# Kernel tuning notes

Hardware: AMD Instinct MI355X
Metric: run time of the kernel (lower is better)

The kernel has to match this reference:

```python
import jax, jax.numpy as jnp
import numpy as np

IN_DIM, MEM_DIM, NUM_WORDS, N_LEAVES = 300, 256, 50000, 8192


def setup_inputs() -> dict:
    key = jax.random.key(0)
    ks = jax.random.split(key, 6)
    s = 0.05
    return {
        "embs": jax.random.normal(ks[0], (N_LEAVES, IN_DIM), jnp.float32),
        "Wx": jax.random.normal(ks[1], (4 * MEM_DIM, IN_DIM), jnp.float32) * s,
        "bx": jax.random.normal(ks[2], (4 * MEM_DIM,), jnp.float32) * s,
        "Wl": jax.random.normal(ks[3], (5 * MEM_DIM, MEM_DIM), jnp.float32) * s,
        "Wr": jax.random.normal(ks[4], (5 * MEM_DIM, MEM_DIM), jnp.float32) * s,
        "emb_table": jax.random.normal(ks[5], (NUM_WORDS, IN_DIM), jnp.float32),
    }


def reference(embs, Wx, bx, Wl, Wr, emb_table):
    m = Wl.shape[1]

    # x-projection order along fused axis: [cx, ix, fx, ox]
    def proj_x(x):  # [B, in] -> [B, 4, m]
        return (x @ Wx.T + bx).reshape(x.shape[0], 4, m)

    # hidden-projection order: [u, i, lf, rf, o]
    def compose(xg, lc, lh, rc, rh):
        lg = (lh @ Wl.T).reshape(-1, 5, m)
        rg = (rh @ Wr.T).reshape(-1, 5, m)
        u = jnp.tanh(xg[:, 0] + lg[:, 0] + rg[:, 0])
        i = jax.nn.sigmoid(xg[:, 1] + lg[:, 1] + rg[:, 1])
        lf = jax.nn.sigmoid(xg[:, 2] + lg[:, 2] + rg[:, 2])  # fx shared
        rf = jax.nn.sigmoid(xg[:, 2] + lg[:, 3] + rg[:, 3])  # fx shared
        c = i * u + lf * lc + rf * rc
        o = jax.nn.sigmoid(xg[:, 3] + lg[:, 4] + rg[:, 4])
        h = o * jnp.tanh(c)
        return c, h

    # leaves: zero child states, per-leaf embedding inputs
    L = embs.shape[0]
    z = jnp.zeros((L, m), embs.dtype)
    c, h = compose(proj_x(embs), z, z, z, z)

    # internal nodes (PAD=True): input is word_embedding(num_words - 1)
    pad_xg = proj_x(emb_table[-1:])  # [1, 4, m]

    while c.shape[0] > 1:  # static shapes; 13 merge levels
        lc, rc = c[0::2], c[1::2]
        lh, rh = h[0::2], h[1::2]
        B = lc.shape[0]
        c, h = compose(jnp.broadcast_to(pad_xg, (B, 4, m)), lc, lh, rc, rh)

    return jnp.stack([c, h])  # root (c, h): [2, 1, mem_dim]
```

## Files before the change

kernel.cpp:

```cpp
#include <hip/hip_runtime.h>
#include <hip/hip_bf16.h>
#include <math.h>


#define MEM 256

typedef __attribute__((ext_vector_type(8))) short bf16x8;
typedef __attribute__((ext_vector_type(4))) float f32x4;

__device__ __forceinline__ float sigf(float x) { return 1.0f / (1.0f + __expf(-x)); }

__device__ __forceinline__ unsigned short f2b(float f) {
  unsigned int u = __float_as_uint(f);
  u = (u + 0x7FFFu + ((u >> 16) & 1u)) >> 16;
  return (unsigned short)u;
}

__device__ __forceinline__ unsigned short cvt1(float f) {
  __hip_bfloat16 b = __float2bfloat16(f);
  return *reinterpret_cast<unsigned short*>(&b);
}

__device__ __forceinline__ bf16x8 gather8(const float* __restrict__ rowp, int k0) {
  bf16x8 r;
  if (k0 + 8 <= 300) {
    const float4 f0 = *(const float4*)(rowp + k0);
    const float4 f1 = *(const float4*)(rowp + k0 + 4);
    r[0] = cvt1(f0.x); r[1] = cvt1(f0.y); r[2] = cvt1(f0.z); r[3] = cvt1(f0.w);
    r[4] = cvt1(f1.x); r[5] = cvt1(f1.y); r[6] = cvt1(f1.z); r[7] = cvt1(f1.w);
  } else {
#pragma unroll
    for (int j = 0; j < 8; j++) {
      int k = k0 + j;
      r[j] = (k < 300) ? (short)cvt1(rowp[k]) : (short)0;
    }
  }
  return r;
}

#define NB_LEAF 1024
#define NB_WCF 2560
__global__ __launch_bounds__(256) void k_fused(
    const float* __restrict__ embs, const float* __restrict__ Wx,
    const float* __restrict__ bx, const float* __restrict__ Wl,
    const float* __restrict__ Wr, const float* __restrict__ emb_last,
    unsigned short* __restrict__ Wcf, float* __restrict__ bias5,
    float* __restrict__ cO, unsigned short* __restrict__ hO) {
  int b = blockIdx.x;
  int tid = threadIdx.x;
  if (b < NB_LEAF) {
    int grp = b & 15, rblk = b >> 4;
    int lane = tid & 63, wave = tid >> 6;
    int tb = (rblk * 4 + wave) * 2;
    int m = lane & 15, quad = lane >> 4;
    const int gmap[3] = {0, 1, 3};

    f32x4 acc[2][3];
#pragma unroll
    for (int rt = 0; rt < 2; rt++)
#pragma unroll
      for (int g = 0; g < 3; g++) acc[rt][g] = (f32x4){0.f, 0.f, 0.f, 0.f};

    const float* ar0 = embs + (tb * 16 + m) * 300;
    const float* ar1 = embs + ((tb + 1) * 16 + m) * 300;
    const float* wr0 = Wx + (gmap[0] * 256 + grp * 16 + m) * 300;
    const float* wr1 = Wx + (gmap[1] * 256 + grp * 16 + m) * 300;
    const float* wr2 = Wx + (gmap[2] * 256 + grp * 16 + m) * 300;
#pragma unroll
    for (int kc = 0; kc < 10; kc++) {
      int k0 = kc * 32 + quad * 8;
      bf16x8 a0 = gather8(ar0, k0);
      bf16x8 a1 = gather8(ar1, k0);
      bf16x8 w0 = gather8(wr0, k0);
      acc[0][0] = __builtin_amdgcn_mfma_f32_16x16x32_bf16(a0, w0, acc[0][0], 0, 0, 0);
      acc[1][0] = __builtin_amdgcn_mfma_f32_16x16x32_bf16(a1, w0, acc[1][0], 0, 0, 0);
      bf16x8 w1 = gather8(wr1, k0);
      acc[0][1] = __builtin_amdgcn_mfma_f32_16x16x32_bf16(a0, w1, acc[0][1], 0, 0, 0);
      acc[1][1] = __builtin_amdgcn_mfma_f32_16x16x32_bf16(a1, w1, acc[1][1], 0, 0, 0);
      bf16x8 w2 = gather8(wr2, k0);
      acc[0][2] = __builtin_amdgcn_mfma_f32_16x16x32_bf16(a0, w2, acc[0][2], 0, 0, 0);
      acc[1][2] = __builtin_amdgcn_mfma_f32_16x16x32_bf16(a1, w2, acc[1][2], 0, 0, 0);
    }
    int col = grp * 16 + m;
    float b0 = bx[col], b1 = bx[256 + col], b3 = bx[768 + col];
#pragma unroll
    for (int rt = 0; rt < 2; rt++) {
#pragma unroll
      for (int reg = 0; reg < 4; reg++) {
        int row = (tb + rt) * 16 + quad * 4 + reg;
        float u = tanhf(acc[rt][0][reg] + b0);
        float ig = sigf(acc[rt][1][reg] + b1);
        float o = sigf(acc[rt][2][reg] + b3);
        float c = ig * u;
        cO[row * MEM + col] = c;
        hO[row * MEM + col] = f2b(o * tanhf(c));
      }
    }
  } else if (b < NB_LEAF + NB_WCF) {
    int idx = (b - NB_LEAF) * 256 + tid;
    int f = idx >> 9, r = idx & 511;
    int lane = r >> 3, j = r & 7;
    int gate = f % 5, t = f / 5;
    int grp = t & 15, kc = t >> 4;
    int k = kc * 32 + ((lane >> 4) << 3) + j;
    int n = gate * 256 + (grp << 4) + (lane & 15);
    float v = (k < 256) ? Wl[n * 256 + k] : Wr[n * 256 + (k - 256)];
    Wcf[idx] = f2b(v);
  } else {
    int g = b - (NB_LEAF + NB_WCF);
    __shared__ float er[300];
    for (int k = tid; k < 300; k += 256) er[k] = emb_last[k];
    __syncthreads();
    const int map[5] = {0, 1, 2, 2, 3};
    int wrow = map[g] * 256 + tid;
    const float* w = Wx + wrow * 300;
    float s = bx[wrow];
    for (int k = 0; k < 300; k++) s += er[k] * w[k];
    bias5[g * 256 + tid] = s;
  }
}

template <int RT>
__global__ __launch_bounds__(256) void k_compose_mfma(
    const unsigned short* __restrict__ hprev,
    const float* __restrict__ cprev,
    const unsigned short* __restrict__ Wcf, const float* __restrict__ bias5,
    float* __restrict__ cO, unsigned short* __restrict__ hO,
    float* __restrict__ hOf, int B) {
  int lane = threadIdx.x & 63;
  int wave = threadIdx.x >> 6;
  int grp = blockIdx.y;
  int tb = (blockIdx.x * 4 + wave) * RT;
  if (tb * 16 >= B) return;
  int m = lane & 15, quad = lane >> 4;
  const bf16x8 zz = {0, 0, 0, 0, 0, 0, 0, 0};

  f32x4 acc[RT][5];
  const unsigned short* ar[RT];
  bool ok[RT];
#pragma unroll
  for (int rt = 0; rt < RT; rt++) {
    int ra = (tb + rt) * 16 + m;
    ok[rt] = (ra < B);
    ar[rt] = hprev + ra * 512 + quad * 8;
#pragma unroll
    for (int g = 0; g < 5; g++) acc[rt][g] = (f32x4){0.f, 0.f, 0.f, 0.f};
  }

#pragma unroll
  for (int kc = 0; kc < 16; kc++) {
    const unsigned short* bp = Wcf + ((kc * 16 + grp) * 5) * 512 + lane * 8;
    bf16x8 b0 = *(const bf16x8*)(bp);
    bf16x8 b1 = *(const bf16x8*)(bp + 512);
    bf16x8 b2 = *(const bf16x8*)(bp + 1024);
    bf16x8 b3 = *(const bf16x8*)(bp + 1536);
    bf16x8 b4 = *(const bf16x8*)(bp + 2048);
#pragma unroll
    for (int rt = 0; rt < RT; rt++) {
      bf16x8 a = ok[rt] ? *(const bf16x8*)(ar[rt] + kc * 32) : zz;
      acc[rt][0] = __builtin_amdgcn_mfma_f32_16x16x32_bf16(a, b0, acc[rt][0], 0, 0, 0);
      acc[rt][1] = __builtin_amdgcn_mfma_f32_16x16x32_bf16(a, b1, acc[rt][1], 0, 0, 0);
      acc[rt][2] = __builtin_amdgcn_mfma_f32_16x16x32_bf16(a, b2, acc[rt][2], 0, 0, 0);
      acc[rt][3] = __builtin_amdgcn_mfma_f32_16x16x32_bf16(a, b3, acc[rt][3], 0, 0, 0);
      acc[rt][4] = __builtin_amdgcn_mfma_f32_16x16x32_bf16(a, b4, acc[rt][4], 0, 0, 0);
    }
  }
  int col = grp * 16 + m;
  float b0 = bias5[col], b1 = bias5[256 + col], b2 = bias5[512 + col];
  float b3 = bias5[768 + col], b4 = bias5[1024 + col];
#pragma unroll
  for (int rt = 0; rt < RT; rt++) {
#pragma unroll
    for (int reg = 0; reg < 4; reg++) {
      int row = (tb + rt) * 16 + quad * 4 + reg;
      if (row >= B) continue;
      float u = tanhf(acc[rt][0][reg] + b0);
      float ig = sigf(acc[rt][1][reg] + b1);
      float lf = sigf(acc[rt][2][reg] + b2);
      float rf = sigf(acc[rt][3][reg] + b3);
      float o = sigf(acc[rt][4][reg] + b4);
      float lc = cprev[(2 * row) * MEM + col];
      float rc = cprev[(2 * row + 1) * MEM + col];
      float c = ig * u + lf * lc + rf * rc;
      float h = o * tanhf(c);
      cO[row * MEM + col] = c;
      hO[row * MEM + col] = f2b(h);
      if (hOf) hOf[row * MEM + col] = h;
    }
  }
}

__global__ __launch_bounds__(256) void k_compose_ksplit(
    const unsigned short* __restrict__ hprev, const float* __restrict__ cprev,
    const unsigned short* __restrict__ Wcf, const float* __restrict__ bias5,
    float* __restrict__ cO, unsigned short* __restrict__ hO,
    float* __restrict__ hOf, int B) {
  __shared__ __align__(16) float lds[4 * 2 * 5 * 64 * 4];
  int tid = threadIdx.x;
  int lane = tid & 63, wave = tid >> 6;
  int grp = blockIdx.y;
  int m = lane & 15, quad = lane >> 4;
  int tiles = (B + 15) >> 4;
  const bf16x8 zz = {0, 0, 0, 0, 0, 0, 0, 0};

  f32x4 acc[2][5];
  bool ok[2];
  const unsigned short* ar[2];
#pragma unroll
  for (int t = 0; t < 2; t++) {
    int ra = t * 16 + m;
    ok[t] = (t < tiles) && (ra < B);
    ar[t] = hprev + ra * 512 + quad * 8;
#pragma unroll
    for (int q = 0; q < 5; q++) acc[t][q] = (f32x4){0.f, 0.f, 0.f, 0.f};
  }

#pragma unroll
  for (int kcl = 0; kcl < 4; kcl++) {
    int kc = wave * 4 + kcl;
    const unsigned short* bp = Wcf + ((kc * 16 + grp) * 5) * 512 + lane * 8;
    bf16x8 b0 = *(const bf16x8*)(bp);
    bf16x8 b1 = *(const bf16x8*)(bp + 512);
    bf16x8 b2 = *(const bf16x8*)(bp + 1024);
    bf16x8 b3 = *(const bf16x8*)(bp + 1536);
    bf16x8 b4 = *(const bf16x8*)(bp + 2048);
#pragma unroll
    for (int t = 0; t < 2; t++) {
      if (t < tiles) {
        bf16x8 a = ok[t] ? *(const bf16x8*)(ar[t] + kc * 32) : zz;
        acc[t][0] = __builtin_amdgcn_mfma_f32_16x16x32_bf16(a, b0, acc[t][0], 0, 0, 0);
        acc[t][1] = __builtin_amdgcn_mfma_f32_16x16x32_bf16(a, b1, acc[t][1], 0, 0, 0);
        acc[t][2] = __builtin_amdgcn_mfma_f32_16x16x32_bf16(a, b2, acc[t][2], 0, 0, 0);
        acc[t][3] = __builtin_amdgcn_mfma_f32_16x16x32_bf16(a, b3, acc[t][3], 0, 0, 0);
        acc[t][4] = __builtin_amdgcn_mfma_f32_16x16x32_bf16(a, b4, acc[t][4], 0, 0, 0);
      }
    }
  }
#pragma unroll
  for (int t = 0; t < 2; t++)
    if (t < tiles)
#pragma unroll
      for (int q = 0; q < 5; q++)
        *(f32x4*)&lds[(((wave * 2 + t) * 5 + q) * 64 + lane) * 4] = acc[t][q];
  __syncthreads();

  if (wave < tiles) {
    int t = wave;
    int col = grp * 16 + m;
    float b0 = bias5[col], b1 = bias5[256 + col], b2 = bias5[512 + col];
    float b3 = bias5[768 + col], b4 = bias5[1024 + col];
    f32x4 s[5];
#pragma unroll
    for (int q = 0; q < 5; q++) {
      s[q] = *(const f32x4*)&lds[(((0 * 2 + t) * 5 + q) * 64 + lane) * 4];
#pragma unroll
      for (int v = 1; v < 4; v++) {
        f32x4 p = *(const f32x4*)&lds[(((v * 2 + t) * 5 + q) * 64 + lane) * 4];
        s[q][0] += p[0]; s[q][1] += p[1]; s[q][2] += p[2]; s[q][3] += p[3];
      }
    }
#pragma unroll
    for (int reg = 0; reg < 4; reg++) {
      int row = t * 16 + quad * 4 + reg;
      if (row >= B) continue;
      float u = tanhf(s[0][reg] + b0);
      float ig = sigf(s[1][reg] + b1);
      float lf = sigf(s[2][reg] + b2);
      float rf = sigf(s[3][reg] + b3);
      float o = sigf(s[4][reg] + b4);
      float lc = cprev[(2 * row) * MEM + col];
      float rc = cprev[(2 * row + 1) * MEM + col];
      float c = ig * u + lf * lc + rf * rc;
      float h = o * tanhf(c);
      cO[row * MEM + col] = c;
      hO[row * MEM + col] = f2b(h);
      if (hOf) hOf[row * MEM + col] = h;
    }
  }
}

extern "C" void kernel_launch(void* const* d_in, const int* in_sizes, int n_in,
                              void* d_out, int out_size, void* d_ws, size_t ws_size,
                              hipStream_t stream) {
  const float* embs = (const float*)d_in[0];
  const float* Wx = (const float*)d_in[1];
  const float* bx = (const float*)d_in[2];
  const float* Wl = (const float*)d_in[3];
  const float* Wr = (const float*)d_in[4];
  const float* emb_table = (const float*)d_in[5];
  float* out = (float*)d_out;

  float* ws = (float*)d_ws;
  float* cA = ws;
  float* cB = cA + 8192 * 256;
  float* bias5 = cB + 4096 * 256;
  unsigned short* hA = (unsigned short*)(bias5 + 1280);
  unsigned short* hB = hA + 8192 * 256;
  unsigned short* Wcf = hB + 4096 * 256;

  k_fused<<<NB_LEAF + NB_WCF + 5, 256, 0, stream>>>(
      embs, Wx, bx, Wl, Wr, emb_table + (in_sizes[5] - 300),
      Wcf, bias5, cA, hA);

  const float* cs = cA;
  const unsigned short* hs = hA;
  int B = 4096;
  int lvl = 0;
  while (B >= 1) {
    float* dc;
    unsigned short* dh;
    float* dhf = nullptr;
    if (B == 1) {
      dc = out;
      dh = hB;
      dhf = out + 256;
    } else if ((lvl & 1) == 0) {
      dc = cB; dh = hB;
    } else {
      dc = cA; dh = hA;
    }
    int tiles = (B + 15) / 16;
    if (B == 4096) {
      k_compose_mfma<2><<<dim3(tiles / 8, 16), 256, 0, stream>>>(
          hs, cs, Wcf, bias5, dc, dh, dhf, B);
    } else if (B >= 64) {
      int gx = (tiles + 3) / 4;
      k_compose_mfma<1><<<dim3(gx, 16), 256, 0, stream>>>(
          hs, cs, Wcf, bias5, dc, dh, dhf, B);
    } else {
      k_compose_ksplit<<<dim3(1, 16), 256, 0, stream>>>(
          hs, cs, Wcf, bias5, dc, dh, dhf, B);
    }
    cs = dc;
    hs = dh;
    B >>= 1;
    lvl++;
  }
}
```

Measured before the change: 265.1 us.

## Pre-convert leaf embeddings and Wx to bf16 fragments, split leaf GEMM kernel, remap block order

The prep kernel now converts embs to a padded bf16 buffer and Wx into MFMA-fragment order, and a separate leaf kernel consumes these with plain vector loads. This replaces the per-block fp32 gather-and-convert, which repeated the conversion of each weight row across many blocks. The Wcf conversion is vectorized to 8 elements per thread. Compose kernels switch to a 1D grid with a sliced block-to-tile remap, likely aimed at cache or XCD locality. The cost is an extra launch plus an extra round trip through memory for the bf16 embedding copy.

Result: faster. 249.3 us (-6.0%).

```diff
diff --git a/kernel.cpp b/kernel.cpp
--- a/kernel.cpp
+++ b/kernel.cpp
@@ -1,5 +1,4 @@
 #include <hip/hip_runtime.h>
-#include <hip/hip_bf16.h>
 #include <math.h>
 
 
@@ -16,98 +15,65 @@
   return (unsigned short)u;
 }
 
-__device__ __forceinline__ unsigned short cvt1(float f) {
-  __hip_bfloat16 b = __float2bfloat16(f);
-  return *reinterpret_cast<unsigned short*>(&b);
-}
-
-__device__ __forceinline__ bf16x8 gather8(const float* __restrict__ rowp, int k0) {
+__device__ __forceinline__ bf16x8 c8(const float* __restrict__ p) {
+  float4 f0 = *(const float4*)(p);
+  float4 f1 = *(const float4*)(p + 4);
   bf16x8 r;
-  if (k0 + 8 <= 300) {
-    const float4 f0 = *(const float4*)(rowp + k0);
-    const float4 f1 = *(const float4*)(rowp + k0 + 4);
-    r[0] = cvt1(f0.x); r[1] = cvt1(f0.y); r[2] = cvt1(f0.z); r[3] = cvt1(f0.w);
-    r[4] = cvt1(f1.x); r[5] = cvt1(f1.y); r[6] = cvt1(f1.z); r[7] = cvt1(f1.w);
-  } else {
-#pragma unroll
-    for (int j = 0; j < 8; j++) {
-      int k = k0 + j;
-      r[j] = (k < 300) ? (short)cvt1(rowp[k]) : (short)0;
-    }
-  }
+  r[0] = (short)f2b(f0.x); r[1] = (short)f2b(f0.y);
+  r[2] = (short)f2b(f0.z); r[3] = (short)f2b(f0.w);
+  r[4] = (short)f2b(f1.x); r[5] = (short)f2b(f1.y);
+  r[6] = (short)f2b(f1.z); r[7] = (short)f2b(f1.w);
   return r;
 }
 
-#define NB_LEAF 1024
-#define NB_WCF 2560
-__global__ __launch_bounds__(256) void k_fused(
+__device__ __forceinline__ bf16x8 g8(const float* __restrict__ rp, int k0) {
+  if (k0 + 8 <= 300) return c8(rp + k0);
+  bf16x8 r;
+#pragma unroll
+  for (int j = 0; j < 8; j++) {
+    int k = k0 + j;
+    r[j] = (k < 300) ? (short)f2b(rp[k]) : (short)0;
+  }
+  return r;
+}
+
+#define NB_EB 1280
+#define NB_WCF 320
+#define NB_WXF 120
+__global__ __launch_bounds__(256) void k_prep(
     const float* __restrict__ embs, const float* __restrict__ Wx,
     const float* __restrict__ bx, const float* __restrict__ Wl,
     const float* __restrict__ Wr, const float* __restrict__ emb_last,
-    unsigned short* __restrict__ Wcf, float* __restrict__ bias5,
-    float* __restrict__ cO, unsigned short* __restrict__ hO) {
-  int b = blockIdx.x;
-  int tid = threadIdx.x;
-  if (b < NB_LEAF) {
-    int grp = b & 15, rblk = b >> 4;
-    int lane = tid & 63, wave = tid >> 6;
-    int tb = (rblk * 4 + wave) * 2;
-    int m = lane & 15, quad = lane >> 4;
-    const int gmap[3] = {0, 1, 3};
-
-    f32x4 acc[2][3];
-#pragma unroll
-    for (int rt = 0; rt < 2; rt++)
-#pragma unroll
-      for (int g = 0; g < 3; g++) acc[rt][g] = (f32x4){0.f, 0.f, 0.f, 0.f};
-
-    const float* ar0 = embs + (tb * 16 + m) * 300;
-    const float* ar1 = embs + ((tb + 1) * 16 + m) * 300;
-    const float* wr0 = Wx + (gmap[0] * 256 + grp * 16 + m) * 300;
-    const float* wr1 = Wx + (gmap[1] * 256 + grp * 16 + m) * 300;
-    const float* wr2 = Wx + (gmap[2] * 256 + grp * 16 + m) * 300;
-#pragma unroll
-    for (int kc = 0; kc < 10; kc++) {
-      int k0 = kc * 32 + quad * 8;
-      bf16x8 a0 = gather8(ar0, k0);
-      bf16x8 a1 = gather8(ar1, k0);
-      bf16x8 w0 = gather8(wr0, k0);
-      acc[0][0] = __builtin_amdgcn_mfma_f32_16x16x32_bf16(a0, w0, acc[0][0], 0, 0, 0);
-      acc[1][0] = __builtin_amdgcn_mfma_f32_16x16x32_bf16(a1, w0, acc[1][0], 0, 0, 0);
-      bf16x8 w1 = gather8(wr1, k0);
-      acc[0][1] = __builtin_amdgcn_mfma_f32_16x16x32_bf16(a0, w1, acc[0][1], 0, 0, 0);
-      acc[1][1] = __builtin_amdgcn_mfma_f32_16x16x32_bf16(a1, w1, acc[1][1], 0, 0, 0);
-      bf16x8 w2 = gather8(wr2, k0);
-      acc[0][2] = __builtin_amdgcn_mfma_f32_16x16x32_bf16(a0, w2, acc[0][2], 0, 0, 0);
-      acc[1][2] = __builtin_amdgcn_mfma_f32_16x16x32_bf16(a1, w2, acc[1][2], 0, 0, 0);
-    }
-    int col = grp * 16 + m;
-    float b0 = bx[col], b1 = bx[256 + col], b3 = bx[768 + col];
-#pragma unroll
-    for (int rt = 0; rt < 2; rt++) {
-#pragma unroll
-      for (int reg = 0; reg < 4; reg++) {
-        int row = (tb + rt) * 16 + quad * 4 + reg;
-        float u = tanhf(acc[rt][0][reg] + b0);
-        float ig = sigf(acc[rt][1][reg] + b1);
-        float o = sigf(acc[rt][2][reg] + b3);
-        float c = ig * u;
-        cO[row * MEM + col] = c;
-        hO[row * MEM + col] = f2b(o * tanhf(c));
-      }
-    }
-  } else if (b < NB_LEAF + NB_WCF) {
-    int idx = (b - NB_LEAF) * 256 + tid;
-    int f = idx >> 9, r = idx & 511;
-    int lane = r >> 3, j = r & 7;
+    unsigned short* __restrict__ eb, unsigned short* __restrict__ Wcf,
+    unsigned short* __restrict__ Wxf, float* __restrict__ bias5) {
+  int b = blockIdx.x, tid = threadIdx.x;
+  if (b < NB_EB) {
+    int idx8 = (b * 256 + tid) * 8;
+    int row = idx8 / 320;
+    int k0 = idx8 - row * 320;
+    *(bf16x8*)(eb + idx8) = g8(embs + row * 300, k0);
+  } else if (b < NB_EB + NB_WCF) {
+    int idx8 = ((b - NB_EB) * 256 + tid) * 8;
+    int f = idx8 >> 9, rr = idx8 & 511;
+    int lane = rr >> 3;
     int gate = f % 5, t = f / 5;
     int grp = t & 15, kc = t >> 4;
-    int k = kc * 32 + ((lane >> 4) << 3) + j;
+    int k0 = kc * 32 + ((lane >> 4) << 3);
     int n = gate * 256 + (grp << 4) + (lane & 15);
-    float v = (k < 256) ? Wl[n * 256 + k] : Wr[n * 256 + (k - 256)];
-    Wcf[idx] = f2b(v);
+    const float* src = (k0 < 256) ? (Wl + n * 256 + k0) : (Wr + n * 256 + (k0 - 256));
+    *(bf16x8*)(Wcf + idx8) = c8(src);
+  } else if (b < NB_EB + NB_WCF + NB_WXF) {
+    int idx8 = ((b - NB_EB - NB_WCF) * 256 + tid) * 8;
+    int f = idx8 >> 9, rr = idx8 & 511;
+    int lane = rr >> 3;
+    int gate = f % 3, t = f / 3;
+    int grp = t & 15, kc = t >> 4;
+    int k0 = kc * 32 + ((lane >> 4) << 3);
+    const int gmap[3] = {0, 1, 3};
+    int n = gmap[gate] * 256 + (grp << 4) + (lane & 15);
+    *(bf16x8*)(Wxf + idx8) = g8(Wx + n * 300, k0);
   } else {
-    int g = b - (NB_LEAF + NB_WCF);
+    int g = b - (NB_EB + NB_WCF + NB_WXF);
     __shared__ float er[300];
     for (int k = tid; k < 300; k += 256) er[k] = emb_last[k];
     __syncthreads();
@@ -120,6 +86,59 @@
   }
 }
 
+__global__ __launch_bounds__(256) void k_leaf_mfma(
+    const unsigned short* __restrict__ eb, const unsigned short* __restrict__ Wxf,
+    const float* __restrict__ bx, float* __restrict__ cO,
+    unsigned short* __restrict__ hO) {
+  int bid = blockIdx.x;
+  int slice = bid & 7, rest = bid >> 3;
+  int rowblock = slice * 8 + (rest & 7);
+  int grp = rest >> 3;
+  int lane = threadIdx.x & 63;
+  int wave = threadIdx.x >> 6;
+  int tb = (rowblock * 4 + wave) * 2;
+  int m = lane & 15, quad = lane >> 4;
+
+  f32x4 acc[2][3];
+#pragma unroll
+  for (int rt = 0; rt < 2; rt++)
+#pragma unroll
+    for (int g = 0; g < 3; g++) acc[rt][g] = (f32x4){0.f, 0.f, 0.f, 0.f};
+
+  const unsigned short* ar0 = eb + (tb * 16 + m) * 320 + quad * 8;
+  const unsigned short* ar1 = eb + ((tb + 1) * 16 + m) * 320 + quad * 8;
+#pragma unroll
+  for (int kc = 0; kc < 10; kc++) {
+    const unsigned short* bp = Wxf + ((kc * 16 + grp) * 3) * 512 + lane * 8;
+    bf16x8 b0 = *(const bf16x8*)(bp);
+    bf16x8 b1 = *(const bf16x8*)(bp + 512);
+    bf16x8 b2 = *(const bf16x8*)(bp + 1024);
+    bf16x8 a0 = *(const bf16x8*)(ar0 + kc * 32);
+    bf16x8 a1 = *(const bf16x8*)(ar1 + kc * 32);
+    acc[0][0] = __builtin_amdgcn_mfma_f32_16x16x32_bf16(a0, b0, acc[0][0], 0, 0, 0);
+    acc[0][1] = __builtin_amdgcn_mfma_f32_16x16x32_bf16(a0, b1, acc[0][1], 0, 0, 0);
+    acc[0][2] = __builtin_amdgcn_mfma_f32_16x16x32_bf16(a0, b2, acc[0][2], 0, 0, 0);
+    acc[1][0] = __builtin_amdgcn_mfma_f32_16x16x32_bf16(a1, b0, acc[1][0], 0, 0, 0);
+    acc[1][1] = __builtin_amdgcn_mfma_f32_16x16x32_bf16(a1, b1, acc[1][1], 0, 0, 0);
+    acc[1][2] = __builtin_amdgcn_mfma_f32_16x16x32_bf16(a1, b2, acc[1][2], 0, 0, 0);
+  }
+  int col = grp * 16 + m;
+  float b0 = bx[col], b1 = bx[256 + col], b3 = bx[768 + col];
+#pragma unroll
+  for (int rt = 0; rt < 2; rt++) {
+#pragma unroll
+    for (int reg = 0; reg < 4; reg++) {
+      int row = (tb + rt) * 16 + quad * 4 + reg;
+      float u = tanhf(acc[rt][0][reg] + b0);
+      float ig = sigf(acc[rt][1][reg] + b1);
+      float o = sigf(acc[rt][2][reg] + b3);
+      float c = ig * u;
+      cO[row * MEM + col] = c;
+      hO[row * MEM + col] = f2b(o * tanhf(c));
+    }
+  }
+}
+
 template <int RT>
 __global__ __launch_bounds__(256) void k_compose_mfma(
     const unsigned short* __restrict__ hprev,
@@ -127,10 +146,18 @@
     const unsigned short* __restrict__ Wcf, const float* __restrict__ bias5,
     float* __restrict__ cO, unsigned short* __restrict__ hO,
     float* __restrict__ hOf, int B) {
+  int tiles = B >> 4;
+  int gx = tiles / (4 * RT);
+  int S = gx >= 8 ? 8 : gx;
+  int pc = gx / S;
+  int bid = blockIdx.x;
+  int slice = bid % S;
+  int rest = bid / S;
+  int rowblock = slice * pc + rest % pc;
+  int grp = rest / pc;
   int lane = threadIdx.x & 63;
   int wave = threadIdx.x >> 6;
-  int grp = blockIdx.y;
-  int tb = (blockIdx.x * 4 + wave) * RT;
+  int tb = (rowblock * 4 + wave) * RT;
   if (tb * 16 >= B) return;
   int m = lane & 15, quad = lane >> 4;
   const bf16x8 zz = {0, 0, 0, 0, 0, 0, 0, 0};
@@ -297,10 +324,14 @@
   unsigned short* hA = (unsigned short*)(bias5 + 1280);
   unsigned short* hB = hA + 8192 * 256;
   unsigned short* Wcf = hB + 4096 * 256;
-
-  k_fused<<<NB_LEAF + NB_WCF + 5, 256, 0, stream>>>(
+  unsigned short* Wxf = Wcf + 1280 * 512;
+  unsigned short* eb = Wxf + 480 * 512;
+
+  k_prep<<<NB_EB + NB_WCF + NB_WXF + 5, 256, 0, stream>>>(
       embs, Wx, bx, Wl, Wr, emb_table + (in_sizes[5] - 300),
-      Wcf, bias5, cA, hA);
+      eb, Wcf, Wxf, bias5);
+
+  k_leaf_mfma<<<1024, 256, 0, stream>>>(eb, Wxf, bx, cA, hA);
 
   const float* cs = cA;
   const unsigned short* hs = hA;
@@ -319,13 +350,13 @@
     } else {
       dc = cA; dh = hA;
     }
-    int tiles = (B + 15) / 16;
     if (B == 4096) {
-      k_compose_mfma<2><<<dim3(tiles / 8, 16), 256, 0, stream>>>(
+      int gx = (B >> 4) / 8;
+      k_compose_mfma<2><<<gx * 16, 256, 0, stream>>>(
           hs, cs, Wcf, bias5, dc, dh, dhf, B);
     } else if (B >= 64) {
-      int gx = (tiles + 3) / 4;
-      k_compose_mfma<1><<<dim3(gx, 16), 256, 0, stream>>>(
+      int gx = (B >> 4) / 4;
+      k_compose_mfma<1><<<gx * 16, 256, 0, stream>>>(
           hs, cs, Wcf, bias5, dc, dh, dhf, B);
     } else {
       k_compose_ksplit<<<dim3(1, 16), 256, 0, stream>>>(
```
